# Optimization experiments

Hardware: AMD Instinct MI355X
Metric: run time of the kernel (lower is better)

## Reference

```python
import jax, jax.numpy as jnp
import numpy as np

N, C, H, W = 8, 192, 112, 112
TEMPERATURE = 0.1


def setup_inputs() -> dict:
    key = jax.random.key(0)
    k1, k2 = jax.random.split(key)
    features = jax.random.normal(k1, (N, C, H, W), dtype=jnp.float32)
    # Raw per-pixel directions in {-1, 0, 1}; clip the neighbor coordinate into
    # bounds and recompute the direction so EVERY neighbor is valid. The torch
    # module's broadcasting (labels[:, i, j] vs an (N, M) gather) only works when
    # all N neighbors are valid at each pixel, so this matches its assumptions.
    raw = jax.random.randint(k2, (N, 2, H, W), -1, 2)
    ii = jnp.arange(H)[None, :, None]
    jj = jnp.arange(W)[None, None, :]
    d0 = jnp.clip(ii + raw[:, 0], 0, H - 1) - ii
    d1 = jnp.clip(jj + raw[:, 1], 0, W - 1) - jj
    directions = jnp.stack([d0, d1], axis=1).astype(jnp.int32)
    # Single-class labels: the original loss is -inf whenever any mask entry is 0
    # (log of exactly 0), so a finite, comparable baseline needs matching labels.
    labels = jnp.zeros((N, H, W), dtype=jnp.int32)
    return {"features": features, "labels": labels, "directions": directions}


def reference(features, labels, directions):
    # F.normalize(features, dim=1): x / max(||x||_2, eps)
    norm = jnp.linalg.norm(features, axis=1, keepdims=True)
    fn = features / jnp.maximum(norm, 1e-12)

    ii = jnp.arange(H)[None, :, None]
    jj = jnp.arange(W)[None, None, :]
    ni = ii + directions[:, 0]  # (N, H, W), in-bounds by construction
    nj = jj + directions[:, 1]  # (N, H, W)

    # Torch: features[:, :, neighbor_i, neighbor_j] gathers the M(==N) neighbor
    # coordinates across ALL batch elements -> (N, C, N, H, W) = [n, c, m, i, j]
    gathered = fn[:, :, ni, nj]
    # logits[n, m, i, j] = <fn[n, :, i, j], fn[n, :, ni[m,i,j], nj[m,i,j]]> / T
    logits = jnp.einsum('ncij,ncmij->nmij', fn, gathered) / TEMPERATURE

    # mask[n, m, i, j] = (labels[m, i, j] == labels[n, ni[m,i,j], nj[m,i,j]])
    # (torch broadcasts labels[:, i, j] along the first axis of the (N, M) gather)
    labels_g = labels[:, ni, nj]  # (N, N, H, W) = [n, m, i, j]
    mask = (labels[None, :, :, :] == labels_g).astype(fn.dtype)

    exp_l = jnp.exp(logits) * mask
    denom = jnp.sum(exp_l, axis=1, keepdims=True)  # sum over m
    # sum_{i,j} mean_{n,m}(.) / (H*W) == global mean over (n, m, i, j)
    loss = (-jnp.log(exp_l / (denom + 1e-6))).mean()
    return loss
```

## Files before the change

kernel.cpp:

```cpp
#include <hip/hip_runtime.h>
#include <math.h>


namespace {
constexpr int N_ = 8, C_ = 192, H_ = 112, W_ = 112;
constexpr int HW = H_ * W_;
constexpr int TH = 7, WS = 28;
constexpr int TROWS = 9, TCOLS = 30;
constexpr int SPAD = 31;
constexpr int TILE_E = TROWS * TCOLS;
constexpr int NT2 = 256;
constexpr int NT = 2 * NT2;
constexpr int EXTRA = TILE_E - NT2;
constexpr int NPR = 4 * WS;
constexpr int CHALF = C_ / 2;
constexpr int KCH = 8;
constexpr int GRP = KCH / 4;
constexpr int NCHUNK = CHALF / KCH;
constexpr int NBLK = (W_ / WS) * (H_ / TH) * N_;
constexpr float INV_T = 10.0f;
constexpr double TOTAL = (double)N_ * N_ * H_ * W_;
}

typedef float v2f __attribute__((ext_vector_type(2)));
typedef float v4f __attribute__((ext_vector_type(4)));

__device__ __forceinline__ void pk(v2f& a, v2f x, v2f y) {
    asm("v_pk_fma_f32 %0, %1, %2, %0" : "+v"(a) : "v"(x), "v"(y));
}
__device__ __forceinline__ void pk4(v2f& a, v4f x, v4f y) {
    pk(a, x.lo, y.lo); pk(a, x.hi, y.hi);
}

__device__ __forceinline__ float sel3(int d, float a, float b, float c) {
    float r = (d < 0) ? a : b;
    return (d > 0) ? c : r;
}

extern "C" __global__ void __launch_bounds__(NT, 4)
dcl_main(const float* __restrict__ feat,
         const int* __restrict__ labels,
         const int* __restrict__ dirs,
         double* __restrict__ partial, int use_partial)
{
    __shared__ v4f   tiles[2][2][GRP][TROWS * SPAD];
    __shared__ float ssp[2][TILE_E];
    __shared__ float ssbuf[TILE_E];
    __shared__ float exA[NPR][9];
    __shared__ float exB[NPR][9];
    __shared__ float red[NT / 64];

    const int bid = blockIdx.x;
    const int n   = bid & 7;
    const int tt  = bid >> 3;
    const int tyb = tt >> 2;
    const int txb = tt & 3;
    const int gy0 = tyb * TH;
    const int gx0 = txb * WS;

    const int tid  = threadIdx.x;
    const int half = tid >> 8;
    const int t8   = tid & (NT2 - 1);

    int gofs0, gofs1 = 0, spad0, spad1 = 0;
    {
        int sr = t8 / TCOLS, sc = t8 - sr * TCOLS;
        spad0 = sr * SPAD + sc;
        gofs0 = min(max(gy0 + sr - 1, 0), H_ - 1) * W_
              + min(max(gx0 + sc - 1, 0), W_ - 1);
        if (t8 < EXTRA) {
            int s2 = t8 + NT2;
            sr = s2 / TCOLS; sc = s2 - sr * TCOLS;
            spad1 = sr * SPAD + sc;
            gofs1 = min(max(gy0 + sr - 1, 0), H_ - 1) * W_
                  + min(max(gx0 + sc - 1, 0), W_ - 1);
        }
    }

    const bool is_p = (t8 < NPR);
    const int pr = t8 / WS;
    const int tx = t8 - pr * WS;
    const int r0 = (pr == 3) ? 5 : 2 * pr;
    const bool px0v = (pr < 3);
    const int top = r0 * SPAD + tx;
    const int gj  = gx0 + tx;

    const float* __restrict__ plane =
        feat + ((size_t)n * C_ + (size_t)half * CHALF) * HW;

    float ss0 = 0.0f, ss1 = 0.0f;

    {
        #pragma unroll
        for (int g = 0; g < GRP; ++g) {
            float a0 = plane[(size_t)(4 * g + 0) * HW + gofs0];
            float a1 = plane[(size_t)(4 * g + 1) * HW + gofs0];
            float a2 = plane[(size_t)(4 * g + 2) * HW + gofs0];
            float a3 = plane[(size_t)(4 * g + 3) * HW + gofs0];
            ss0 += a0 * a0 + a1 * a1 + a2 * a2 + a3 * a3;
            v4f v = {a0, a1, a2, a3};
            tiles[half][0][g][spad0] = v;
        }
        if (t8 < EXTRA) {
            #pragma unroll
            for (int g = 0; g < GRP; ++g) {
                float a0 = plane[(size_t)(4 * g + 0) * HW + gofs1];
                float a1 = plane[(size_t)(4 * g + 1) * HW + gofs1];
                float a2 = plane[(size_t)(4 * g + 2) * HW + gofs1];
                float a3 = plane[(size_t)(4 * g + 3) * HW + gofs1];
                ss1 += a0 * a0 + a1 * a1 + a2 * a2 + a3 * a3;
                v4f v = {a0, a1, a2, a3};
                tiles[half][0][g][spad1] = v;
            }
        }
    }
    __syncthreads();

    v2f q0[7], q1[7], s01;
    {
        const v2f z = {0.f, 0.f};
        #pragma unroll
        for (int d = 0; d < 7; ++d) { q0[d] = z; q1[d] = z; }
        s01 = z;
    }

    for (int t = 0; t < NCHUNK; ++t) {
        float pv0[KCH], pv1[KCH];
        const bool more = (t + 1 < NCHUNK);
        if (more) {
            const float* p = plane + (size_t)(t + 1) * KCH * HW;
            #pragma unroll
            for (int k = 0; k < KCH; ++k) pv0[k] = p[(size_t)k * HW + gofs0];
            if (t8 < EXTRA) {
                #pragma unroll
                for (int k = 0; k < KCH; ++k) pv1[k] = p[(size_t)k * HW + gofs1];
            }
        }

        if (is_p) {
            #pragma unroll
            for (int g = 0; g < GRP; ++g) {
                const v4f* __restrict__ cp = tiles[half][t & 1][g];
                v4f A0 = cp[top +  0], B0 = cp[top +  1], C0 = cp[top +  2];
                v4f A1 = cp[top + 31], B1 = cp[top + 32], C1 = cp[top + 33];
                v4f A2 = cp[top + 62], B2 = cp[top + 63], C2 = cp[top + 64];
                pk4(q0[0], B1, A0); pk4(q0[1], B1, B0); pk4(q0[2], B1, C0);
                pk4(q0[3], B1, A1); pk4(q0[4], B1, C1);
                pk4(q0[5], B1, A2); pk4(s01,   B1, B2); pk4(q0[6], B1, C2);
                v4f A3 = cp[top + 93], B3 = cp[top + 94], C3 = cp[top + 95];
                pk4(q1[0], B2, A1); pk4(q1[1], B2, C1);
                pk4(q1[2], B2, A2); pk4(q1[3], B2, C2);
                pk4(q1[4], B2, A3); pk4(q1[5], B2, B3); pk4(q1[6], B2, C3);
            }
        }

        if (more) {
            const int nb = (t + 1) & 1;
            #pragma unroll
            for (int g = 0; g < GRP; ++g) {
                float a0 = pv0[4 * g + 0], a1 = pv0[4 * g + 1];
                float a2 = pv0[4 * g + 2], a3 = pv0[4 * g + 3];
                ss0 += a0 * a0 + a1 * a1 + a2 * a2 + a3 * a3;
                v4f v = {a0, a1, a2, a3};
                tiles[half][nb][g][spad0] = v;
            }
            if (t8 < EXTRA) {
                #pragma unroll
                for (int g = 0; g < GRP; ++g) {
                    float a0 = pv1[4 * g + 0], a1 = pv1[4 * g + 1];
                    float a2 = pv1[4 * g + 2], a3 = pv1[4 * g + 3];
                    ss1 += a0 * a0 + a1 * a1 + a2 * a2 + a3 * a3;
                    v4f v = {a0, a1, a2, a3};
                    tiles[half][nb][g][spad1] = v;
                }
            }
            __syncthreads();
        }
    }

    ssp[half][t8] = ss0;
    if (t8 < EXTRA) ssp[half][t8 + NT2] = ss1;
    if (is_p) {
        if (half == 1) {
            float* d = exA[t8];
            d[0]=q0[0].x+q0[0].y; d[1]=q0[1].x+q0[1].y; d[2]=q0[2].x+q0[2].y;
            d[3]=q0[3].x+q0[3].y; d[4]=q0[4].x+q0[4].y; d[5]=q0[5].x+q0[5].y;
            d[6]=s01.x+s01.y;     d[7]=q0[6].x+q0[6].y;
        } else {
            float* d = exB[t8];
            d[0]=q1[0].x+q1[0].y; d[1]=s01.x+s01.y;     d[2]=q1[1].x+q1[1].y;
            d[3]=q1[2].x+q1[2].y; d[4]=q1[3].x+q1[3].y; d[5]=q1[4].x+q1[4].y;
            d[6]=q1[5].x+q1[5].y; d[7]=q1[6].x+q1[6].y;
        }
    }
    __syncthreads();
    if (tid < TILE_E)
        ssbuf[tid] = 1.0f / fmaxf(sqrtf(ssp[0][tid] + ssp[1][tid]), 1e-12f);
    __syncthreads();

    float lp = 0.0f;
    if (is_p) {
        auto epi = [&](const float* s8, int ciu, int gi) -> float {
            const float ssq = ssp[0][ciu] + ssp[1][ciu];
            const float invc = ssbuf[ciu] * INV_T;
            const float l00 = s8[0] * invc * ssbuf[ciu - TCOLS - 1];
            const float l01 = s8[1] * invc * ssbuf[ciu - TCOLS];
            const float l02 = s8[2] * invc * ssbuf[ciu - TCOLS + 1];
            const float l10 = s8[3] * invc * ssbuf[ciu - 1];
            const float l11 = ssq  * invc * ssbuf[ciu];
            const float l12 = s8[4] * invc * ssbuf[ciu + 1];
            const float l20 = s8[5] * invc * ssbuf[ciu + TCOLS - 1];
            const float l21 = s8[6] * invc * ssbuf[ciu + TCOLS];
            const float l22 = s8[7] * invc * ssbuf[ciu + TCOLS + 1];

            const int pix = gi * W_ + gj;
            float denom = 0.f, sumlog = 0.f;
            #pragma unroll
            for (int m = 0; m < N_; ++m) {
                int d0 = dirs[((m * 2 + 0) * H_ + gi) * W_ + gj];
                int d1 = dirs[((m * 2 + 1) * H_ + gi) * W_ + gj];
                float e0 = sel3(d1, l00, l01, l02);
                float e1 = sel3(d1, l10, l11, l12);
                float e2 = sel3(d1, l20, l21, l22);
                float lm = sel3(d0, e0, e1, e2);
                int labm = labels[m * HW + pix];
                int labn = labels[n * HW + (gi + d0) * W_ + (gj + d1)];
                bool msk = (labm == labn);
                float e = msk ? __expf(lm) : 0.f;
                denom += e;
                sumlog += msk ? lm : -INFINITY;
            }
            return 8.0f * __logf(denom + 1e-6f) - sumlog;
        };

        if (half == 0) {
            if (px0v) {
                float f[8];
                const float* e = exA[t8];
                f[0]=q0[0].x+q0[0].y+e[0]; f[1]=q0[1].x+q0[1].y+e[1];
                f[2]=q0[2].x+q0[2].y+e[2]; f[3]=q0[3].x+q0[3].y+e[3];
                f[4]=q0[4].x+q0[4].y+e[4]; f[5]=q0[5].x+q0[5].y+e[5];
                f[6]=s01.x+s01.y+e[6];     f[7]=q0[6].x+q0[6].y+e[7];
                lp = epi(f, (r0 + 1) * TCOLS + tx + 1, gy0 + r0);
            }
        } else {
            float f[8];
            const float* e = exB[t8];
            f[0]=q1[0].x+q1[0].y+e[0]; f[1]=s01.x+s01.y+e[1];
            f[2]=q1[1].x+q1[1].y+e[2]; f[3]=q1[2].x+q1[2].y+e[3];
            f[4]=q1[3].x+q1[3].y+e[4]; f[5]=q1[4].x+q1[4].y+e[5];
            f[6]=q1[5].x+q1[5].y+e[6]; f[7]=q1[6].x+q1[6].y+e[7];
            lp = epi(f, (r0 + 2) * TCOLS + tx + 1, gy0 + r0 + 1);
        }
    }

    #pragma unroll
    for (int off = 32; off > 0; off >>= 1) lp += __shfl_down(lp, off, 64);
    const int wave = tid >> 6, lane = tid & 63;
    if (lane == 0) red[wave] = lp;
    __syncthreads();
    if (tid == 0) {
        float tsum = 0.f;
        #pragma unroll
        for (int w = 0; w < NT / 64; ++w) tsum += red[w];
        if (use_partial) partial[bid] = (double)tsum;
        else atomicAdd(partial, (double)tsum);
    }
}

extern "C" __global__ void __launch_bounds__(256)
dcl_final(const double* __restrict__ partial, float* __restrict__ out, int nblk)
{
    const int tid = threadIdx.x;
    double s = 0.0;
    for (int i = tid; i < nblk; i += 256) s += partial[i];
    #pragma unroll
    for (int off = 32; off > 0; off >>= 1) s += __shfl_down(s, off, 64);
    __shared__ double red[4];
    const int lane = tid & 63, wv = tid >> 6;
    if (lane == 0) red[wv] = s;
    __syncthreads();
    if (tid == 0) out[0] = (float)((red[0] + red[1] + red[2] + red[3]) / TOTAL);
}

extern "C" void kernel_launch(void* const* d_in, const int* in_sizes, int n_in,
                              void* d_out, int out_size, void* d_ws, size_t ws_size,
                              hipStream_t stream) {
    const float* feat   = (const float*)d_in[0];
    const int*   labels = (const int*)d_in[1];
    const int*   dirs   = (const int*)d_in[2];
    double* acc = (double*)d_ws;
    float*  out = (float*)d_out;

    const int use_partial = (ws_size >= (size_t)NBLK * sizeof(double)) ? 1 : 0;
    if (!use_partial) hipMemsetAsync(acc, 0, sizeof(double), stream);
    dcl_main<<<dim3(NBLK), NT, 0, stream>>>(feat, labels, dirs, acc, use_partial);
    dcl_final<<<1, 256, 0, stream>>>(acc, out, use_partial ? NBLK : 1);
}
```

Measured before the change: 121.6 us.

## Use 14x14 square tiles and fuse final reduction via last-block atomic counter

```diff
diff --git a/kernel.cpp b/kernel.cpp
--- a/kernel.cpp
+++ b/kernel.cpp
@@ -5,19 +5,18 @@
 namespace {
 constexpr int N_ = 8, C_ = 192, H_ = 112, W_ = 112;
 constexpr int HW = H_ * W_;
-constexpr int TH = 7, WS = 28;
-constexpr int TROWS = 9, TCOLS = 30;
-constexpr int SPAD = 31;
-constexpr int TILE_E = TROWS * TCOLS;
+constexpr int TH = 14, WS = 14;
+constexpr int TCOLS = 16;
+constexpr int TPAD = 17;
+constexpr int TILE_E = 256;
 constexpr int NT2 = 256;
 constexpr int NT = 2 * NT2;
-constexpr int EXTRA = TILE_E - NT2;
-constexpr int NPR = 4 * WS;
+constexpr int NPR = 7 * WS;
 constexpr int CHALF = C_ / 2;
 constexpr int KCH = 8;
 constexpr int GRP = KCH / 4;
 constexpr int NCHUNK = CHALF / KCH;
-constexpr int NBLK = (W_ / WS) * (H_ / TH) * N_;
+constexpr int NBLK = 8 * 8 * 8;
 constexpr float INV_T = 10.0f;
 constexpr double TOTAL = (double)N_ * N_ * H_ * W_;
 }
@@ -41,77 +40,50 @@
 dcl_main(const float* __restrict__ feat,
          const int* __restrict__ labels,
          const int* __restrict__ dirs,
-         double* __restrict__ partial, int use_partial)
+         double* __restrict__ acc,
+         float* __restrict__ out)
 {
-    __shared__ v4f   tiles[2][2][GRP][TROWS * SPAD];
+    __shared__ v4f   tiles[2][2][GRP][16 * TPAD];
     __shared__ float ssp[2][TILE_E];
     __shared__ float ssbuf[TILE_E];
     __shared__ float exA[NPR][9];
     __shared__ float exB[NPR][9];
     __shared__ float red[NT / 64];
 
-    const int bid = blockIdx.x;
-    const int n   = bid & 7;
-    const int tt  = bid >> 3;
-    const int tyb = tt >> 2;
-    const int txb = tt & 3;
-    const int gy0 = tyb * TH;
-    const int gx0 = txb * WS;
+    const int gx0 = blockIdx.x * WS;
+    const int gy0 = blockIdx.y * TH;
+    const int n   = blockIdx.z;
 
     const int tid  = threadIdx.x;
     const int half = tid >> 8;
     const int t8   = tid & (NT2 - 1);
 
-    int gofs0, gofs1 = 0, spad0, spad1 = 0;
-    {
-        int sr = t8 / TCOLS, sc = t8 - sr * TCOLS;
-        spad0 = sr * SPAD + sc;
-        gofs0 = min(max(gy0 + sr - 1, 0), H_ - 1) * W_
-              + min(max(gx0 + sc - 1, 0), W_ - 1);
-        if (t8 < EXTRA) {
-            int s2 = t8 + NT2;
-            sr = s2 / TCOLS; sc = s2 - sr * TCOLS;
-            spad1 = sr * SPAD + sc;
-            gofs1 = min(max(gy0 + sr - 1, 0), H_ - 1) * W_
-                  + min(max(gx0 + sc - 1, 0), W_ - 1);
-        }
-    }
+    const int sr = t8 >> 4, sc = t8 & 15;
+    const int spad = sr * TPAD + sc;
+    const int gofs = min(max(gy0 + sr - 1, 0), H_ - 1) * W_
+                   + min(max(gx0 + sc - 1, 0), W_ - 1);
 
     const bool is_p = (t8 < NPR);
     const int pr = t8 / WS;
     const int tx = t8 - pr * WS;
-    const int r0 = (pr == 3) ? 5 : 2 * pr;
-    const bool px0v = (pr < 3);
-    const int top = r0 * SPAD + tx;
+    const int top = (2 * pr) * TPAD + tx;
     const int gj  = gx0 + tx;
 
     const float* __restrict__ plane =
         feat + ((size_t)n * C_ + (size_t)half * CHALF) * HW;
 
-    float ss0 = 0.0f, ss1 = 0.0f;
+    float ss0 = 0.0f;
 
     {
         #pragma unroll
         for (int g = 0; g < GRP; ++g) {
-            float a0 = plane[(size_t)(4 * g + 0) * HW + gofs0];
-            float a1 = plane[(size_t)(4 * g + 1) * HW + gofs0];
-            float a2 = plane[(size_t)(4 * g + 2) * HW + gofs0];
-            float a3 = plane[(size_t)(4 * g + 3) * HW + gofs0];
+            float a0 = plane[(size_t)(4 * g + 0) * HW + gofs];
+            float a1 = plane[(size_t)(4 * g + 1) * HW + gofs];
+            float a2 = plane[(size_t)(4 * g + 2) * HW + gofs];
+            float a3 = plane[(size_t)(4 * g + 3) * HW + gofs];
             ss0 += a0 * a0 + a1 * a1 + a2 * a2 + a3 * a3;
             v4f v = {a0, a1, a2, a3};
-            tiles[half][0][g][spad0] = v;
-        }
-        if (t8 < EXTRA) {
-            #pragma unroll
-            for (int g = 0; g < GRP; ++g) {
-                float a0 = plane[(size_t)(4 * g + 0) * HW + gofs1];
-                float a1 = plane[(size_t)(4 * g + 1) * HW + gofs1];
-                float a2 = plane[(size_t)(4 * g + 2) * HW + gofs1];
-                float a3 = plane[(size_t)(4 * g + 3) * HW + gofs1];
-                ss1 += a0 * a0 + a1 * a1 + a2 * a2 + a3 * a3;
-                v4f v = {a0, a1, a2, a3};
-                tiles[half][0][g][spad1] = v;
-            }
+            tiles[half][0][g][spad] = v;
         }
     }
     __syncthreads();
@@ -125,16 +97,12 @@
     }
 
     for (int t = 0; t < NCHUNK; ++t) {
-        float pv0[KCH], pv1[KCH];
+        float pv[KCH];
         const bool more = (t + 1 < NCHUNK);
         if (more) {
             const float* p = plane + (size_t)(t + 1) * KCH * HW;
             #pragma unroll
-            for (int k = 0; k < KCH; ++k) pv0[k] = p[(size_t)k * HW + gofs0];
-            if (t8 < EXTRA) {
-                #pragma unroll
-                for (int k = 0; k < KCH; ++k) pv1[k] = p[(size_t)k * HW + gofs1];
-            }
+            for (int k = 0; k < KCH; ++k) pv[k] = p[(size_t)k * HW + gofs];
         }
 
         if (is_p) {
@@ -142,12 +110,12 @@
             for (int g = 0; g < GRP; ++g) {
                 const v4f* __restrict__ cp = tiles[half][t & 1][g];
                 v4f A0 = cp[top +  0], B0 = cp[top +  1], C0 = cp[top +  2];
-                v4f A1 = cp[top + 31], B1 = cp[top + 32], C1 = cp[top + 33];
-                v4f A2 = cp[top + 62], B2 = cp[top + 63], C2 = cp[top + 64];
+                v4f A1 = cp[top + 17], B1 = cp[top + 18], C1 = cp[top + 19];
+                v4f A2 = cp[top + 34], B2 = cp[top + 35], C2 = cp[top + 36];
                 pk4(q0[0], B1, A0); pk4(q0[1], B1, B0); pk4(q0[2], B1, C0);
                 pk4(q0[3], B1, A1); pk4(q0[4], B1, C1);
                 pk4(q0[5], B1, A2); pk4(s01,   B1, B2); pk4(q0[6], B1, C2);
-                v4f A3 = cp[top + 93], B3 = cp[top + 94], C3 = cp[top + 95];
+                v4f A3 = cp[top + 51], B3 = cp[top + 52], C3 = cp[top + 53];
                 pk4(q1[0], B2, A1); pk4(q1[1], B2, C1);
                 pk4(q1[2], B2, A2); pk4(q1[3], B2, C2);
                 pk4(q1[4], B2, A3); pk4(q1[5], B2, B3); pk4(q1[6], B2, C3);
@@ -158,28 +126,17 @@
             const int nb = (t + 1) & 1;
             #pragma unroll
             for (int g = 0; g < GRP; ++g) {
-                float a0 = pv0[4 * g + 0], a1 = pv0[4 * g + 1];
-                float a2 = pv0[4 * g + 2], a3 = pv0[4 * g + 3];
+                float a0 = pv[4 * g + 0], a1 = pv[4 * g + 1];
+                float a2 = pv[4 * g + 2], a3 = pv[4 * g + 3];
                 ss0 += a0 * a0 + a1 * a1 + a2 * a2 + a3 * a3;
                 v4f v = {a0, a1, a2, a3};
-                tiles[half][nb][g][spad0] = v;
-            }
-            if (t8 < EXTRA) {
-                #pragma unroll
-                for (int g = 0; g < GRP; ++g) {
-                    float a0 = pv1[4 * g + 0], a1 = pv1[4 * g + 1];
-                    float a2 = pv1[4 * g + 2], a3 = pv1[4 * g + 3];
-                    ss1 += a0 * a0 + a1 * a1 + a2 * a2 + a3 * a3;
-                    v4f v = {a0, a1, a2, a3};
-                    tiles[half][nb][g][spad1] = v;
-                }
+                tiles[half][nb][g][spad] = v;
             }
             __syncthreads();
         }
     }
 
     ssp[half][t8] = ss0;
-    if (t8 < EXTRA) ssp[half][t8 + NT2] = ss1;
     if (is_p) {
         if (half == 1) {
             float* d = exA[t8];
@@ -234,15 +191,13 @@
         };
 
         if (half == 0) {
-            if (px0v) {
-                float f[8];
-                const float* e = exA[t8];
-                f[0]=q0[0].x+q0[0].y+e[0]; f[1]=q0[1].x+q0[1].y+e[1];
-                f[2]=q0[2].x+q0[2].y+e[2]; f[3]=q0[3].x+q0[3].y+e[3];
-                f[4]=q0[4].x+q0[4].y+e[4]; f[5]=q0[5].x+q0[5].y+e[5];
-                f[6]=s01.x+s01.y+e[6];     f[7]=q0[6].x+q0[6].y+e[7];
-                lp = epi(f, (r0 + 1) * TCOLS + tx + 1, gy0 + r0);
-            }
+            float f[8];
+            const float* e = exA[t8];
+            f[0]=q0[0].x+q0[0].y+e[0]; f[1]=q0[1].x+q0[1].y+e[1];
+            f[2]=q0[2].x+q0[2].y+e[2]; f[3]=q0[3].x+q0[3].y+e[3];
+            f[4]=q0[4].x+q0[4].y+e[4]; f[5]=q0[5].x+q0[5].y+e[5];
+            f[6]=s01.x+s01.y+e[6];     f[7]=q0[6].x+q0[6].y+e[7];
+            lp = epi(f, (2 * pr + 1) * TCOLS + tx + 1, gy0 + 2 * pr);
         } else {
             float f[8];
             const float* e = exB[t8];
@@ -250,7 +205,7 @@
             f[2]=q1[1].x+q1[1].y+e[2]; f[3]=q1[2].x+q1[2].y+e[3];
             f[4]=q1[3].x+q1[3].y+e[4]; f[5]=q1[4].x+q1[4].y+e[5];
             f[6]=q1[5].x+q1[5].y+e[6]; f[7]=q1[6].x+q1[6].y+e[7];
-            lp = epi(f, (r0 + 2) * TCOLS + tx + 1, gy0 + r0 + 1);
+            lp = epi(f, (2 * pr + 2) * TCOLS + tx + 1, gy0 + 2 * pr + 1);
         }
     }
 
@@ -263,24 +218,16 @@
         float tsum = 0.f;
         #pragma unroll
         for (int w = 0; w < NT / 64; ++w) tsum += red[w];
-        if (use_partial) partial[bid] = (double)tsum;
-        else atomicAdd(partial, (double)tsum);
-    }
-}
-
-extern "C" __global__ void __launch_bounds__(256)
-dcl_final(const double* __restrict__ partial, float* __restrict__ out, int nblk)
-{
-    const int tid = threadIdx.x;
-    double s = 0.0;
-    for (int i = tid; i < nblk; i += 256) s += partial[i];
-    #pragma unroll
-    for (int off = 32; off > 0; off >>= 1) s += __shfl_down(s, off, 64);
-    __shared__ double red[4];
-    const int lane = tid & 63, wv = tid >> 6;
-    if (lane == 0) red[wv] = s;
-    __syncthreads();
-    if (tid == 0) out[0] = (float)((red[0] + red[1] + red[2] + red[3]) / TOTAL);
+        atomicAdd(acc, (double)tsum);
+        __threadfence();
+        unsigned* ctr = (unsigned*)(acc + 1);
+        unsigned old = atomicAdd(ctr, 1u);
+        if (old == (unsigned)(NBLK - 1)) {
+            __threadfence();
+            double s = atomicAdd(acc, 0.0);
+            out[0] = (float)(s / TOTAL);
+        }
+    }
 }
 
 extern "C" void kernel_launch(void* const* d_in, const int* in_sizes, int n_in,
@@ -292,8 +239,7 @@
     double* acc = (double*)d_ws;
     float*  out = (float*)d_out;
 
-    const int use_partial = (ws_size >= (size_t)NBLK * sizeof(double)) ? 1 : 0;
-    if (!use_partial) hipMemsetAsync(acc, 0, sizeof(double), stream);
-    dcl_main<<<dim3(NBLK), NT, 0, stream>>>(feat, labels, dirs, acc, use_partial);
-    dcl_final<<<1, 256, 0, stream>>>(acc, out, use_partial ? NBLK : 1);
-}
+    hipMemsetAsync(acc, 0, 16, stream);
+    dim3 grid(W_ / WS, H_ / TH, N_);
+    dcl_main<<<grid, NT, 0, stream>>>(feat, labels, dirs, acc, out);
+}
```

After: 138.8 us. 1.14x slower.

## Deepen global-load prefetch to two chunks and use a custom LDS-only barrier

Applied to the files above, without the earlier changes.

```diff
diff --git a/kernel.cpp b/kernel.cpp
--- a/kernel.cpp
+++ b/kernel.cpp
@@ -37,6 +37,13 @@
     return (d > 0) ? c : r;
 }
 
+#define BAR() do {                                            \
+    asm volatile("s_waitcnt lgkmcnt(0)" ::: "memory");        \
+    __builtin_amdgcn_sched_barrier(0);                        \
+    __builtin_amdgcn_s_barrier();                             \
+    __builtin_amdgcn_sched_barrier(0);                        \
+} while (0)
+
 extern "C" __global__ void __launch_bounds__(NT, 4)
 dcl_main(const float* __restrict__ feat,
          const int* __restrict__ labels,
@@ -52,9 +59,9 @@
 
     const int bid = blockIdx.x;
     const int n   = bid & 7;
-    const int tt  = bid >> 3;
-    const int tyb = tt >> 2;
-    const int txb = tt & 3;
+    const int tt_ = bid >> 3;
+    const int tyb = tt_ >> 2;
+    const int txb = tt_ & 3;
     const int gy0 = tyb * TH;
     const int gx0 = txb * WS;
 
@@ -90,32 +97,6 @@
 
     float ss0 = 0.0f, ss1 = 0.0f;
 
-    {
-        #pragma unroll
-        for (int g = 0; g < GRP; ++g) {
-            float a0 = plane[(size_t)(4 * g + 0) * HW + gofs0];
-            float a1 = plane[(size_t)(4 * g + 1) * HW + gofs0];
-            float a2 = plane[(size_t)(4 * g + 2) * HW + gofs0];
-            float a3 = plane[(size_t)(4 * g + 3) * HW + gofs0];
-            ss0 += a0 * a0 + a1 * a1 + a2 * a2 + a3 * a3;
-            v4f v = {a0, a1, a2, a3};
-            tiles[half][0][g][spad0] = v;
-        }
-        if (t8 < EXTRA) {
-            #pragma unroll
-            for (int g = 0; g < GRP; ++g) {
-                float a0 = plane[(size_t)(4 * g + 0) * HW + gofs1];
-                float a1 = plane[(size_t)(4 * g + 1) * HW + gofs1];
-                float a2 = plane[(size_t)(4 * g + 2) * HW + gofs1];
-                float a3 = plane[(size_t)(4 * g + 3) * HW + gofs1];
-                ss1 += a0 * a0 + a1 * a1 + a2 * a2 + a3 * a3;
-                v4f v = {a0, a1, a2, a3};
-                tiles[half][0][g][spad1] = v;
-            }
-        }
-    }
-    __syncthreads();
-
     v2f q0[7], q1[7], s01;
     {
         const v2f z = {0.f, 0.f};
@@ -124,18 +105,44 @@
         s01 = z;
     }
 
-    for (int t = 0; t < NCHUNK; ++t) {
-        float pv0[KCH], pv1[KCH];
-        const bool more = (t + 1 < NCHUNK);
-        if (more) {
-            const float* p = plane + (size_t)(t + 1) * KCH * HW;
-            #pragma unroll
-            for (int k = 0; k < KCH; ++k) pv0[k] = p[(size_t)k * HW + gofs0];
-            if (t8 < EXTRA) {
-                #pragma unroll
-                for (int k = 0; k < KCH; ++k) pv1[k] = p[(size_t)k * HW + gofs1];
-            }
-        }
+    float pvA0[KCH], pvA1[KCH], pvB0[KCH], pvB1[KCH];
+
+    auto writebuf = [&](int nb, const float (&h0)[KCH], const float (&h1)[KCH]) {
+        #pragma unroll
+        for (int g = 0; g < GRP; ++g) {
+            float a0 = h0[4*g+0], a1 = h0[4*g+1], a2 = h0[4*g+2], a3 = h0[4*g+3];
+            ss0 += a0*a0 + a1*a1 + a2*a2 + a3*a3;
+            v4f v = {a0, a1, a2, a3};
+            tiles[half][nb][g][spad0] = v;
+        }
+        if (t8 < EXTRA) {
+            #pragma unroll
+            for (int g = 0; g < GRP; ++g) {
+                float a0 = h1[4*g+0], a1 = h1[4*g+1], a2 = h1[4*g+2], a3 = h1[4*g+3];
+                ss1 += a0*a0 + a1*a1 + a2*a2 + a3*a3;
+                v4f v = {a0, a1, a2, a3};
+                tiles[half][nb][g][spad1] = v;
+            }
+        }
+    };
+    auto loadch = [&](int c, float (&f0)[KCH], float (&f1)[KCH]) {
+        const float* p = plane + (size_t)c * KCH * HW;
+        #pragma unroll
+        for (int k = 0; k < KCH; ++k) f0[k] = p[(size_t)k * HW + gofs0];
+        if (t8 < EXTRA) {
+            #pragma unroll
+            for (int k = 0; k < KCH; ++k) f1[k] = p[(size_t)k * HW + gofs1];
+        }
+    };
+
+    loadch(0, pvB0, pvB1);
+    loadch(1, pvA0, pvA1);
+    writebuf(0, pvB0, pvB1);
+    BAR();
+
+    auto step = [&](int t, float (&h0)[KCH], float (&h1)[KCH],
+                           float (&f0)[KCH], float (&f1)[KCH]) {
+        if (t + 2 < NCHUNK) loadch(t + 2, f0, f1);
 
         if (is_p) {
             #pragma unroll
@@ -154,28 +161,15 @@
             }
         }
 
-        if (more) {
-            const int nb = (t + 1) & 1;
-            #pragma unroll
-            for (int g = 0; g < GRP; ++g) {
-                float a0 = pv0[4 * g + 0], a1 = pv0[4 * g + 1];
-                float a2 = pv0[4 * g + 2], a3 = pv0[4 * g + 3];
-                ss0 += a0 * a0 + a1 * a1 + a2 * a2 + a3 * a3;
-                v4f v = {a0, a1, a2, a3};
-                tiles[half][nb][g][spad0] = v;
-            }
-            if (t8 < EXTRA) {
-                #pragma unroll
-                for (int g = 0; g < GRP; ++g) {
-                    float a0 = pv1[4 * g + 0], a1 = pv1[4 * g + 1];
-                    float a2 = pv1[4 * g + 2], a3 = pv1[4 * g + 3];
-                    ss1 += a0 * a0 + a1 * a1 + a2 * a2 + a3 * a3;
-                    v4f v = {a0, a1, a2, a3};
-                    tiles[half][nb][g][spad1] = v;
-                }
-            }
-            __syncthreads();
-        }
+        if (t + 1 < NCHUNK) {
+            writebuf((t + 1) & 1, h0, h1);
+            BAR();
+        }
+    };
+
+    for (int tt = 0; tt < NCHUNK; tt += 2) {
+        step(tt,     pvA0, pvA1, pvB0, pvB1);
+        step(tt + 1, pvB0, pvB1, pvA0, pvA1);
     }
 
     ssp[half][t8] = ss0;
```

New measurement: 123.1 us. No clear change (+1.2%).
